# Performance work log

Measured on AMD Instinct MI355X. Metric: run time of the kernel, lower is better.

## Reference

```python
import jax, jax.numpy as jnp
import numpy as np
from jax import lax

EPS = 1e-5

def _ternarize_impl(w):
    # TWN: delta = 0.7*mean|w|; alpha = mean(|w| over |w|>delta); w -> {-alpha,0,+alpha}
    abs_w = jnp.abs(w)
    delta = 0.7 * abs_w.mean()
    mask_pos = w > delta
    mask_neg = w < -delta
    nz = mask_pos | mask_neg
    cnt = nz.sum()
    alpha = jnp.where(cnt > 0, (abs_w * nz).sum() / jnp.maximum(cnt, 1).astype(w.dtype), abs_w.mean())
    return jnp.where(mask_pos, alpha, jnp.where(mask_neg, -alpha, jnp.zeros((), w.dtype)))

def ternarize(w):
    return _ternarize_impl(w)

def conv_block(x, w, b, gamma, beta):
    tw = ternarize(w)
    y = lax.conv_general_dilated(x, tw, window_strides=(1, 1),
                                 padding=((1, 1), (1, 1)),
                                 dimension_numbers=('NCHW', 'OIHW', 'NCHW'))
    y = y + b[None, :, None, None]
    # BatchNorm2d in training mode: batch statistics over (N,H,W)
    mean = y.mean(axis=(0, 2, 3), keepdims=True)
    var = y.var(axis=(0, 2, 3), keepdims=True)
    y = (y - mean) * lax.rsqrt(var + EPS)
    y = y * gamma[None, :, None, None] + beta[None, :, None, None]
    y = jax.nn.relu(y)
    # MaxPool2d(2)
    y = lax.reduce_window(y, -jnp.inf, lax.max, (1, 1, 2, 2), (1, 1, 2, 2), 'VALID')
    return y

def setup_inputs() -> dict:
    key = jax.random.key(0)
    ks = jax.random.split(key, 32)
    chans = [3, 64, 128, 256, 512]
    d = {"x": jax.random.normal(ks[0], (32, 3, 128, 128), jnp.float32)}
    for i in range(4):
        cin, cout = chans[i], chans[i + 1]
        fan = cin * 9
        d[f"w{i+1}"] = jax.random.normal(ks[1 + 3 * i], (cout, cin, 3, 3), jnp.float32) / np.sqrt(fan)
        d[f"b{i+1}"] = jax.random.normal(ks[2 + 3 * i], (cout,), jnp.float32) * 0.01
        d[f"g{i+1}"] = jnp.ones((cout,), jnp.float32)
        d[f"be{i+1}"] = jnp.zeros((cout,), jnp.float32)
    fc_in = 512 * 8 * 8  # spatial = 128 // 2**4 = 8
    d["fw1"] = jax.random.normal(ks[20], (1024, fc_in), jnp.float32) / np.sqrt(fc_in)
    d["fb1"] = jax.random.normal(ks[21], (1024,), jnp.float32) * 0.01
    d["fw2"] = jax.random.normal(ks[22], (1000, 1024), jnp.float32) / np.sqrt(1024)
    d["fb2"] = jax.random.normal(ks[23], (1000,), jnp.float32) * 0.01
    return d

def reference(x, w1, b1, g1, be1, w2, b2, g2, be2, w3, b3, g3, be3, w4, b4, g4, be4, fw1, fb1, fw2, fb2):
    y = conv_block(x, w1, b1, g1, be1)
    y = conv_block(y, w2, b2, g2, be2)
    y = conv_block(y, w3, b3, g3, be3)
    y = conv_block(y, w4, b4, g4, be4)
    y = y.reshape(y.shape[0], -1)  # [B, 512*8*8]
    y = y @ ternarize(fw1).T + fb1
    y = jax.nn.relu(y)
    y = y @ ternarize(fw2).T + fb2
    return y
```

## Files before the change

kernel.cpp:

```cpp
#include <hip/hip_runtime.h>
#include <hip/hip_bf16.h>
#include <stdint.h>

#define DEV __device__ __forceinline__

typedef __bf16 bf16x8 __attribute__((ext_vector_type(8)));
typedef float f32x4 __attribute__((ext_vector_type(4)));
typedef unsigned short us8 __attribute__((ext_vector_type(8)));
typedef int8_t i8x8 __attribute__((ext_vector_type(8)));

DEV unsigned short f2us(float f) {
  __hip_bfloat16 h = __float2bfloat16(f);
  unsigned short u;
  __builtin_memcpy(&u, &h, 2);
  return u;
}

DEV double wave_reduce_d(double v) {
#pragma unroll
  for (int off = 32; off > 0; off >>= 1) v += __shfl_down(v, off);
  return v;
}

DEV double dbl_block_reduce(double v, double* lds) {
  v = wave_reduce_d(v);
  int lane = threadIdx.x & 63, w = threadIdx.x >> 6;
  if (lane == 0) lds[w] = v;
  __syncthreads();
  double r = 0.0;
  if (threadIdx.x == 0) r = lds[0] + lds[1] + lds[2] + lds[3];
  __syncthreads();
  return r;
}

struct TDesc { const float* w; int n; int b0; int nb; int slot; };
struct TDescs { TDesc d[6]; };

DEV double abs4d(float4 v) {
  return fabs((double)v.x) + fabs((double)v.y) + fabs((double)v.z) + fabs((double)v.w);
}

DEV double bucket_sum64(const double* b) {
  double s = 0.0;
#pragma unroll
  for (int j = 0; j < 64; ++j) s += b[j];
  return s;
}

__global__ __launch_bounds__(256) void tern_abs_all(TDescs td, double* __restrict__ absB) {
  __shared__ double lds[4];
  const int b = blockIdx.x;
  int k = 0;
  while (k < 5 && b >= td.d[k + 1].b0) ++k;
  const TDesc D = td.d[k];
  const float4* w4 = (const float4*)D.w;
  const int n4 = D.n >> 2;
  const int S = D.nb * 256;
  int i = (b - D.b0) * 256 + threadIdx.x;
  double s0 = 0.0, s1 = 0.0, s2 = 0.0, s3 = 0.0;
  for (; i + 3 * S < n4; i += 4 * S) {
    float4 v0 = w4[i];
    float4 v1 = w4[i + S];
    float4 v2 = w4[i + 2 * S];
    float4 v3 = w4[i + 3 * S];
    s0 += abs4d(v0);
    s1 += abs4d(v1);
    s2 += abs4d(v2);
    s3 += abs4d(v3);
  }
  for (; i < n4; i += S) s0 += abs4d(w4[i]);
  double s = (s0 + s1) + (s2 + s3);
  s = dbl_block_reduce(s, lds);
  if (threadIdx.x == 0 && s != 0.0) atomicAdd(absB + D.slot * 64 + (b & 63), s);
}

struct MDesc { const float* w; int8_t* out; int n; int b0; int nb; int slot; };
struct MDescs { MDesc d[6]; };

DEV int proc4(float4 v, double delta, double& ms, int& cnt) {
  float e[4] = {v.x, v.y, v.z, v.w};
  char pk[4];
#pragma unroll
  for (int j = 0; j < 4; ++j) {
    double d = (double)e[j];
    double a = fabs(d);
    if (a > delta) { ms += a; cnt += 1; }
    pk[j] = (char)((d > delta) ? 1 : ((d < -delta) ? -1 : 0));
  }
  int w32;
  __builtin_memcpy(&w32, pk, 4);
  return w32;
}

__global__ __launch_bounds__(256) void tern_masked_code_all(MDescs td,
                                                            const double* __restrict__ absB,
                                                            double* __restrict__ msB,
                                                            double* __restrict__ cntB) {
  __shared__ double lds[4];
  const int b = blockIdx.x;
  int k = 0;
  while (k < 5 && b >= td.d[k + 1].b0) ++k;
  const MDesc D = td.d[k];
  const float4* w4 = (const float4*)D.w;
  int8_t* out = D.out;
  const int n4 = D.n >> 2;
  const double delta = 0.7 * bucket_sum64(absB + D.slot * 64) / (double)D.n;
  const int S = D.nb * 256;
  int i = (b - D.b0) * 256 + threadIdx.x;
  double m0 = 0.0, m1 = 0.0, m2 = 0.0, m3 = 0.0;
  int c0 = 0, c1x = 0, c2x = 0, c3 = 0;
  for (; i + 3 * S < n4; i += 4 * S) {
    float4 v0 = w4[i];
    float4 v1 = w4[i + S];
    float4 v2 = w4[i + 2 * S];
    float4 v3 = w4[i + 3 * S];
    int p0 = proc4(v0, delta, m0, c0);
    int p1 = proc4(v1, delta, m1, c1x);
    int p2 = proc4(v2, delta, m2, c2x);
    int p3 = proc4(v3, delta, m3, c3);
    if (out) {
      *(int*)(out + ((size_t)i << 2)) = p0;
      *(int*)(out + ((size_t)(i + S) << 2)) = p1;
      *(int*)(out + ((size_t)(i + 2 * S) << 2)) = p2;
      *(int*)(out + ((size_t)(i + 3 * S) << 2)) = p3;
    }
  }
  for (; i < n4; i += S) {
    int p = proc4(w4[i], delta, m0, c0);
    if (out) *(int*)(out + ((size_t)i << 2)) = p;
  }
  double ms = (m0 + m1) + (m2 + m3);
  double cnt = (double)(c0 + c1x + c2x + c3);
  ms = dbl_block_reduce(ms, lds);
  cnt = dbl_block_reduce(cnt, lds);
  if (threadIdx.x == 0 && cnt != 0.0) {
    atomicAdd(msB + D.slot * 64 + (b & 63), ms);
    atomicAdd(cntB + D.slot * 64 + (b & 63), cnt);
  }
}

__global__ __launch_bounds__(64) void tern_collapse(const double* __restrict__ absB,
                                                    const double* __restrict__ msB,
                                                    const double* __restrict__ cntB,
                                                    double* __restrict__ st) {
  const int t = blockIdx.x;
  const int lane = threadIdx.x;
  double a = absB[t * 64 + lane];
  double m = msB[t * 64 + lane];
  double c = cntB[t * 64 + lane];
#pragma unroll
  for (int off = 32; off > 0; off >>= 1) {
    a += __shfl_down(a, off);
    m += __shfl_down(m, off);
    c += __shfl_down(c, off);
  }
  if (lane == 0) {
    st[t * 4] = a;
    st[t * 4 + 1] = m;
    st[t * 4 + 2] = c;
  }
}

DEV float tern_alpha_d(const double* st, double n) {
  double cnt = st[2];
  return (float)(cnt > 0.0 ? st[1] / fmax(cnt, 1.0) : st[0] / n);
}
DEV double tern_alpha_dd(const double* st, double n) {
  double cnt = st[2];
  return cnt > 0.0 ? st[1] / fmax(cnt, 1.0) : st[0] / n;
}

__global__ __launch_bounds__(256) void tern_write_convb(const float* __restrict__ w,
                                                        const double* __restrict__ ab, int total,
                                                        int CIN, unsigned short* __restrict__ out) {
  int i = blockIdx.x * 256 + threadIdx.x;
  if (i >= total) return;
  double delta = 0.7 * bucket_sum64(ab) / (double)total;
  double v = (double)w[i];
  float code = v > delta ? 1.f : (v < -delta ? -1.f : 0.f);
  int cin9 = CIN * 9;
  int o = i / cin9, rem = i - o * cin9;
  int ci = rem / 9, tap = rem - ci * 9;
  int CH = CIN >> 5;
  int blk = o >> 7, cop = o & 127;
  int wv = cop >> 5, g = (cop >> 4) & 1, l15 = cop & 15;
  int cc = ci >> 5, l4 = (ci >> 3) & 3, j = ci & 7;
  size_t idx =
      (((((size_t)(blk * CH + cc) * 9 + tap) * 4 + wv) * 2 + g) * 64 + l4 * 16 + l15) * 8 + j;
  out[idx] = f2us(code);
}

__global__ __launch_bounds__(256) void tern_write_convb_pad(const float* __restrict__ w,
                                                            const double* __restrict__ ab,
                                                            unsigned short* __restrict__ out) {
  int i = blockIdx.x * 256 + threadIdx.x;
  if (i >= 64 * 32) return;
  int o = i >> 5, k = i & 31;
  float code = 0.f;
  if (k < 27) {
    int dy = k / 9, r = k - dy * 9, dx = r / 3, ci = r - dx * 3;
    int tap = dy * 3 + dx;
    double delta = 0.7 * bucket_sum64(ab) / 1728.0;
    double v = (double)w[(o * 3 + ci) * 9 + tap];
    code = v > delta ? 1.f : (v < -delta ? -1.f : 0.f);
  }
  out[i] = f2us(code);
}

__global__ __launch_bounds__(256) void bn_fin_alpha(const double* __restrict__ pS,
                                                    const double* __restrict__ pQ, int P,
                                                    const float* __restrict__ g,
                                                    const float* __restrict__ be, double M,
                                                    const double* __restrict__ st, double nels,
                                                    float* __restrict__ scsh, int C) {
  __shared__ double lds[4];
  const int c = blockIdx.x;
  double s = 0.0, q = 0.0;
  for (int p = threadIdx.x; p < P; p += 256) {
    s += pS[(size_t)p * C + c];
    q += pQ[(size_t)p * C + c];
  }
  s = dbl_block_reduce(s, lds);
  q = dbl_block_reduce(q, lds);
  if (threadIdx.x == 0) {
    double al = tern_alpha_dd(st, nels);
    double mean = s / M;
    double var = q / M - mean * mean;
    double sc = (double)g[c] * al / sqrt(al * al * var + 1e-5);
    scsh[c] = (float)sc;
    scsh[C + c] = (float)((double)be[c] - mean * sc);
  }
}

DEV void cvt8(float4 a, float4 b, us8& hv, us8& lv) {
  float f[8] = {a.x, a.y, a.z, a.w, b.x, b.y, b.z, b.w};
#pragma unroll
  for (int e = 0; e < 8; ++e) {
    __hip_bfloat16 h = __float2bfloat16(f[e]);
    unsigned short hu;
    __builtin_memcpy(&hu, &h, 2);
    hv[e] = hu;
    lv[e] = f2us(f[e] - __bfloat162float(h));
  }
}

template <int PH>
DEV void bn_partials(const f32x4 (&acc)[2][PH], int wvCout, int CO, int p,
                     double* __restrict__ pS, double* __restrict__ pQ) {
  const int lane = threadIdx.x & 63;
  const int l15 = lane & 15, l4 = lane >> 4;
#pragma unroll
  for (int g = 0; g < 2; ++g) {
    float sv[4] = {0, 0, 0, 0}, qv[4] = {0, 0, 0, 0};
#pragma unroll
    for (int pt = 0; pt < PH; ++pt)
#pragma unroll
      for (int r = 0; r < 4; ++r) {
        float v = acc[g][pt][r];
        sv[r] += v;
        qv[r] = fmaf(v, v, qv[r]);
      }
#pragma unroll
    for (int r = 0; r < 4; ++r)
#pragma unroll
      for (int m = 1; m < 16; m <<= 1) {
        sv[r] += __shfl_xor(sv[r], m);
        qv[r] += __shfl_xor(qv[r], m);
      }
    if (l15 == 0) {
#pragma unroll
      for (int r = 0; r < 4; ++r) {
        int co = wvCout + g * 16 + l4 * 4 + r;
        pS[(size_t)p * CO + co] = (double)sv[r];
        pQ[(size_t)p * CO + co] = (double)qv[r];
      }
    }
  }
}

template <int CIN, int PH>
DEV void mfma_phase(const unsigned short* __restrict__ wT, const unsigned short* hC,
                    const unsigned short* lC, int wv, int blk, int cc, int lane,
                    f32x4 (&acc)[2][PH]) {
  constexpr int CH = CIN / 32;
  const int l15 = lane & 15, l4 = lane >> 4;
#pragma unroll
  for (int tap = 0; tap < 9; ++tap) {
    const int dy = tap / 3, dx = tap % 3;
    bf16x8 aF[2];
    const size_t wbase = (((size_t)(blk * CH + cc) * 9 + tap) * 4 + wv) * 2;
#pragma unroll
    for (int g = 0; g < 2; ++g)
      aF[g] = *(const bf16x8*)(wT + (wbase + g) * 512 + lane * 8);
    const int tb = (dy * 18 + dx + l15) * 32 + l4 * 8;
#pragma unroll
    for (int pt = 0; pt < PH; ++pt) {
      int off = tb + pt * (18 * 32);
      bf16x8 bh = *(const bf16x8*)(hC + off);
      bf16x8 bl = *(const bf16x8*)(lC + off);
      acc[0][pt] = __builtin_amdgcn_mfma_f32_16x16x32_bf16(aF[0], bh, acc[0][pt], 0, 0, 0);
      acc[1][pt] = __builtin_amdgcn_mfma_f32_16x16x32_bf16(aF[1], bh, acc[1][pt], 0, 0, 0);
      acc[0][pt] = __builtin_amdgcn_mfma_f32_16x16x32_bf16(aF[0], bl, acc[0][pt], 0, 0, 0);
      acc[1][pt] = __builtin_amdgcn_mfma_f32_16x16x32_bf16(aF[1], bl, acc[1][pt], 0, 0, 0);
    }
  }
}

template <int CIN, int H, int PH>
__global__ __launch_bounds__(256) void conv_mfma(const float* __restrict__ inNHWC,
                                                 const unsigned short* __restrict__ wT,
                                                 float* __restrict__ z, int COUT,
                                                 double* __restrict__ pS,
                                                 double* __restrict__ pQ) {
  constexpr int W = H;
  constexpr int CH = CIN / 32;
  constexpr int TX = W / 16;
  constexpr int NU = (PH + 2) * 18 * 4;
  constexpr int T = 256;
  constexpr int UPT = (NU + T - 1) / T;
  constexpr int TILE = (PH + 2) * 18 * 32;
  __shared__ unsigned short hiT[TILE];
  __shared__ unsigned short loT[TILE];
  const int bx = blockIdx.x;
  const int tX = bx % TX, tY = bx / TX;
  const int n = blockIdx.z;
  const int wave = threadIdx.x >> 6, lane = threadIdx.x & 63;
  const int l15 = lane & 15, l4 = lane >> 4;
  const int wvCout = blockIdx.y * 128 + wave * 32;
  const int x0 = tX * 16, y0 = tY * PH;

  f32x4 acc[2][PH];
#pragma unroll
  for (int g = 0; g < 2; ++g)
#pragma unroll
    for (int pt = 0; pt < PH; ++pt) acc[g][pt] = (f32x4){0.f, 0.f, 0.f, 0.f};

  const float* srcB[UPT];
  int ldsO[UPT];
  bool inb[UPT];
#pragma unroll
  for (int j = 0; j < UPT; ++j) {
    int u = threadIdx.x + j * T;
    int q = u & 3, rem = u >> 2;
    int xx = rem % 18, yy = rem / 18;
    int gy = y0 + yy - 1, gx = x0 + xx - 1;
    bool ok = (u < NU) && ((unsigned)gy < (unsigned)H) && ((unsigned)gx < (unsigned)W);
    inb[j] = ok;
    int cy = ok ? gy : 0, cx = ok ? gx : 0;
    srcB[j] = inNHWC + (((size_t)(n * H + cy) * W + cx) * CIN + q * 8);
    ldsO[j] = (rem << 5) + (q << 3);
  }
  float4 pa[UPT], pb[UPT];
#pragma unroll
  for (int j = 0; j < UPT; ++j)
    if (inb[j]) {
      pa[j] = *(const float4*)srcB[j];
      pb[j] = *(const float4*)(srcB[j] + 4);
    }
#pragma unroll 1
  for (int cc = 0; cc < CH; ++cc) {
    if (cc) {
      asm volatile("s_waitcnt lgkmcnt(0)" ::: "memory");
      __builtin_amdgcn_s_barrier();
      __builtin_amdgcn_sched_barrier(0);
    }
#pragma unroll
    for (int j = 0; j < UPT; ++j) {
      int u = threadIdx.x + j * T;
      if (u < NU) {
        us8 hv = (us8)0, lv = (us8)0;
        if (inb[j]) cvt8(pa[j], pb[j], hv, lv);
        *(us8*)(hiT + ldsO[j]) = hv;
        *(us8*)(loT + ldsO[j]) = lv;
      }
    }
    asm volatile("s_waitcnt lgkmcnt(0)" ::: "memory");
    __builtin_amdgcn_s_barrier();
    __builtin_amdgcn_sched_barrier(0);
    if (cc + 1 < CH) {
#pragma unroll
      for (int j = 0; j < UPT; ++j)
        if (inb[j]) {
          pa[j] = *(const float4*)(srcB[j] + (size_t)(cc + 1) * 32);
          pb[j] = *(const float4*)(srcB[j] + (size_t)(cc + 1) * 32 + 4);
        }
    }
    mfma_phase<CIN, PH>(wT, hiT, loT, wave, blockIdx.y, cc, lane, acc);
  }

#pragma unroll
  for (int g = 0; g < 2; ++g)
#pragma unroll
    for (int pt = 0; pt < PH; ++pt) {
      int oy = y0 + pt;
#pragma unroll
      for (int r = 0; r < 4; ++r) {
        int co = wvCout + g * 16 + l4 * 4 + r;
        z[(((size_t)n * COUT + co) * H + oy) * W + x0 + l15] = acc[g][pt][r];
      }
    }
  bn_partials<PH>(acc, wvCout, COUT, n * gridDim.x + bx, pS, pQ);
}

DEV void conv1_core(const float* __restrict__ x, const unsigned short* __restrict__ wb,
                    int n, int x0, int y0, float* xt, f32x4 (&acc)[2][8]) {
  const int lane = threadIdx.x & 63;
  const int l15 = lane & 15, l4 = lane >> 4;
  const int wvCout = (threadIdx.x >> 6) * 32;
#pragma unroll
  for (int g = 0; g < 2; ++g)
#pragma unroll
    for (int pt = 0; pt < 8; ++pt) acc[g][pt] = (f32x4){0.f, 0.f, 0.f, 0.f};

  for (int u = threadIdx.x; u < 540; u += 128) {
    int yy = u / 54, rem = u - yy * 54;
    int tx = rem / 3, ci = rem - tx * 3;
    int gy = y0 + yy - 1, gx = x0 + tx - 1;
    float v = 0.f;
    if ((unsigned)gy < 128u && (unsigned)gx < 128u)
      v = x[(((size_t)n * 3 + ci) << 14) + (gy << 7) + gx];
    xt[u] = v;
  }
  asm volatile("s_waitcnt lgkmcnt(0)" ::: "memory");
  __builtin_amdgcn_s_barrier();
  __builtin_amdgcn_sched_barrier(0);

  bf16x8 aW[2];
#pragma unroll
  for (int g = 0; g < 2; ++g)
    aW[g] = *(const bf16x8*)(wb + (size_t)(wvCout + g * 16 + l15) * 32 + l4 * 8);

#pragma unroll
  for (int pt = 0; pt < 8; ++pt) {
    us8 hv = (us8)0, lv = (us8)0;
#pragma unroll
    for (int j = 0; j < 8; ++j) {
      int k = l4 * 8 + j;
      float v = 0.f;
      if (k < 27) {
        int dy = k / 9;
        int r = k - dy * 9;
        v = xt[(pt + dy) * 54 + l15 * 3 + r];
      }
      __hip_bfloat16 h = __float2bfloat16(v);
      unsigned short hu;
      __builtin_memcpy(&hu, &h, 2);
      hv[j] = hu;
      lv[j] = f2us(v - __bfloat162float(h));
    }
    bf16x8 bh, bl;
    __builtin_memcpy(&bh, &hv, 16);
    __builtin_memcpy(&bl, &lv, 16);
    acc[0][pt] = __builtin_amdgcn_mfma_f32_16x16x32_bf16(aW[0], bh, acc[0][pt], 0, 0, 0);
    acc[0][pt] = __builtin_amdgcn_mfma_f32_16x16x32_bf16(aW[0], bl, acc[0][pt], 0, 0, 0);
    acc[1][pt] = __builtin_amdgcn_mfma_f32_16x16x32_bf16(aW[1], bh, acc[1][pt], 0, 0, 0);
    acc[1][pt] = __builtin_amdgcn_mfma_f32_16x16x32_bf16(aW[1], bl, acc[1][pt], 0, 0, 0);
  }
}

__global__ __launch_bounds__(128) void conv1_mfma_stats(const float* __restrict__ x,
                                                        const unsigned short* __restrict__ wT,
                                                        double* __restrict__ pS,
                                                        double* __restrict__ pQ) {
  __shared__ float xt[540];
  const int bx = blockIdx.x;
  const int tX = bx & 7, tY = bx >> 3;
  const int n = blockIdx.z;
  f32x4 acc[2][8];
  conv1_core(x, wT, n, tX * 16, tY * 8, xt, acc);
  bn_partials<8>(acc, (threadIdx.x >> 6) * 32, 64, n * gridDim.x + bx, pS, pQ);
}

__global__ __launch_bounds__(128) void conv1_mfma_pool(const float* __restrict__ x,
                                                       const unsigned short* __restrict__ wT,
                                                       const float* __restrict__ scsh,
                                                       float* __restrict__ outNHWC) {
  __shared__ float xt[540];
  const int bx = blockIdx.x;
  const int tX = bx & 7, tY = bx >> 3;
  const int n = blockIdx.z;
  const int lane = threadIdx.x & 63;
  const int l15 = lane & 15, l4 = lane >> 4;
  const int wvCout = (threadIdx.x >> 6) * 32;
  const int x0 = tX * 16, y0 = tY * 8;
  f32x4 acc[2][8];
  conv1_core(x, wT, n, x0, y0, xt, acc);
#pragma unroll
  for (int g = 0; g < 2; ++g) {
    const int co0 = wvCout + g * 16 + l4 * 4;
#pragma unroll
    for (int pt = 0; pt < 8; pt += 2) {
      float m[4];
#pragma unroll
      for (int r = 0; r < 4; ++r) {
        float sc = scsh[co0 + r], sh = scsh[64 + co0 + r];
        float v0 = fmaxf(fmaf(acc[g][pt][r], sc, sh), 0.f);
        float v1 = fmaxf(fmaf(acc[g][pt + 1][r], sc, sh), 0.f);
        float a = fmaxf(v0, v1);
        m[r] = fmaxf(a, __shfl_xor(a, 1));
      }
      if ((l15 & 1) == 0) {
        int oy = (y0 + pt) >> 1, ox = (x0 + l15) >> 1;
        *(float4*)(outNHWC + ((((size_t)n * 64 + oy) * 64 + ox) << 6) + co0) =
            make_float4(m[0], m[1], m[2], m[3]);
      }
    }
  }
}

__global__ __launch_bounds__(256) void bn_pool_nhwc(const float* __restrict__ z,
                                                    const float* __restrict__ scsh, int C,
                                                    int lw, float* __restrict__ out) {
  __shared__ float t[64][65];
  const int Wo = 1 << lw, Wi = Wo << 1;
  const int c0 = blockIdx.x * 64, p0 = blockIdx.y * 64, n = blockIdx.z;
  const int NP = Wo * Wo;
  for (int u = threadIdx.x; u < 4096; u += 256) {
    int cl = u >> 6, pl = u & 63;
    int pp = p0 + pl, ho = pp >> lw, wo = pp & (Wo - 1);
    int c = c0 + cl;
    size_t idx = ((size_t)(n * C + c) * Wi + (ho << 1)) * Wi + (wo << 1);
    float sc = scsh[c], sh = scsh[C + c];
    float z00 = fmaxf(fmaf(z[idx], sc, sh), 0.f);
    float z01 = fmaxf(fmaf(z[idx + 1], sc, sh), 0.f);
    float z10 = fmaxf(fmaf(z[idx + Wi], sc, sh), 0.f);
    float z11 = fmaxf(fmaf(z[idx + Wi + 1], sc, sh), 0.f);
    t[cl][pl] = fmaxf(fmaxf(z00, z01), fmaxf(z10, z11));
  }
  __syncthreads();
  for (int u = threadIdx.x; u < 4096; u += 256) {
    int pl = u >> 6, cl = u & 63;
    out[((size_t)n * NP + p0 + pl) * C + c0 + cl] = t[cl][pl];
  }
}

__global__ __launch_bounds__(256) void bn_pool_hilo(const float* __restrict__ z,
                                                    const float* __restrict__ scsh,
                                                    unsigned short* __restrict__ hi,
                                                    unsigned short* __restrict__ lo) {
  int i = blockIdx.x * 256 + threadIdx.x;
  int wo = i & 7, ho = (i >> 3) & 7, c = (i >> 6) & 511, n = i >> 15;
  float sc = scsh[c], sh = scsh[512 + c];
  size_t idx = ((size_t)(n * 512 + c) * 16 + (ho << 1)) * 16 + (wo << 1);
  float z00 = fmaxf(fmaf(z[idx], sc, sh), 0.f);
  float z01 = fmaxf(fmaf(z[idx + 1], sc, sh), 0.f);
  float z10 = fmaxf(fmaf(z[idx + 16], sc, sh), 0.f);
  float z11 = fmaxf(fmaf(z[idx + 17], sc, sh), 0.f);
  float f = fmaxf(fmaxf(z00, z01), fmaxf(z10, z11));
  __hip_bfloat16 h = __float2bfloat16(f);
  unsigned short hu;
  __builtin_memcpy(&hu, &h, 2);
  hi[i] = hu;
  lo[i] = f2us(f - __bfloat162float(h));
}

DEV bf16x8 i8_to_bf16x8(i8x8 v) {
  us8 u;
#pragma unroll
  for (int j = 0; j < 8; ++j) {
    int c = v[j];
    u[j] = (unsigned short)(c == 0 ? 0 : (c > 0 ? 0x3F80 : 0xBF80));
  }
  bf16x8 r;
  __builtin_memcpy(&r, &u, 16);
  return r;
}

__global__ __launch_bounds__(256) void fc1_mfma(const int8_t* __restrict__ c1,
                                                const unsigned short* __restrict__ aHi,
                                                const unsigned short* __restrict__ aLo,
                                                float* __restrict__ partial) {
  const int w = threadIdx.x >> 6, lane = threadIdx.x & 63;
  const int l15 = lane & 15, l4 = lane >> 4;
  const int o0 = blockIdx.x * 128 + w * 32;
  const int s = blockIdx.y;
  const int kbase = s * 256 + l4 * 8;
  f32x4 acc[2][2];
#pragma unroll
  for (int g = 0; g < 2; ++g)
#pragma unroll
    for (int t = 0; t < 2; ++t) acc[g][t] = (f32x4){0.f, 0.f, 0.f, 0.f};
#pragma unroll 2
  for (int kc = 0; kc < 256; kc += 32) {
    bf16x8 a0 = i8_to_bf16x8(*(const i8x8*)(c1 + (size_t)(o0 + l15) * 32768 + kbase + kc));
    bf16x8 a1 = i8_to_bf16x8(*(const i8x8*)(c1 + (size_t)(o0 + 16 + l15) * 32768 + kbase + kc));
    bf16x8 bh0 = *(const bf16x8*)(aHi + (size_t)l15 * 32768 + kbase + kc);
    bf16x8 bl0 = *(const bf16x8*)(aLo + (size_t)l15 * 32768 + kbase + kc);
    bf16x8 bh1 = *(const bf16x8*)(aHi + (size_t)(16 + l15) * 32768 + kbase + kc);
    bf16x8 bl1 = *(const bf16x8*)(aLo + (size_t)(16 + l15) * 32768 + kbase + kc);
    acc[0][0] = __builtin_amdgcn_mfma_f32_16x16x32_bf16(a0, bh0, acc[0][0], 0, 0, 0);
    acc[0][0] = __builtin_amdgcn_mfma_f32_16x16x32_bf16(a0, bl0, acc[0][0], 0, 0, 0);
    acc[1][0] = __builtin_amdgcn_mfma_f32_16x16x32_bf16(a1, bh0, acc[1][0], 0, 0, 0);
    acc[1][0] = __builtin_amdgcn_mfma_f32_16x16x32_bf16(a1, bl0, acc[1][0], 0, 0, 0);
    acc[0][1] = __builtin_amdgcn_mfma_f32_16x16x32_bf16(a0, bh1, acc[0][1], 0, 0, 0);
    acc[0][1] = __builtin_amdgcn_mfma_f32_16x16x32_bf16(a0, bl1, acc[0][1], 0, 0, 0);
    acc[1][1] = __builtin_amdgcn_mfma_f32_16x16x32_bf16(a1, bh1, acc[1][1], 0, 0, 0);
    acc[1][1] = __builtin_amdgcn_mfma_f32_16x16x32_bf16(a1, bl1, acc[1][1], 0, 0, 0);
  }
#pragma unroll
  for (int g = 0; g < 2; ++g)
#pragma unroll
    for (int t = 0; t < 2; ++t)
#pragma unroll
      for (int r = 0; r < 4; ++r) {
        int o = o0 + g * 16 + l4 * 4 + r;
        int n = t * 16 + l15;
        partial[((size_t)s * 1024 + o) * 32 + n] = acc[g][t][r];
      }
}

__global__ __launch_bounds__(256) void fc1_fin(const float* __restrict__ partial,
                                               const double* __restrict__ st,
                                               const float* __restrict__ fb,
                                               float* __restrict__ fc1T) {
  int i = blockIdx.x * 256 + threadIdx.x;
  int o = i >> 5;
  float s = 0.f;
#pragma unroll 8
  for (int t = 0; t < 128; ++t) s += partial[(size_t)t * 32768 + i];
  float alpha = tern_alpha_d(st, 33554432.0);
  fc1T[i] = fmaxf(fmaf(s, alpha, fb[o]), 0.f);
}

__global__ __launch_bounds__(256) void fc2_kernel(const float* __restrict__ xT,
                                                  const int8_t* __restrict__ codes,
                                                  const double* __restrict__ st,
                                                  const float* __restrict__ fb,
                                                  float* __restrict__ out) {
  const int o = blockIdx.x;
  float acc[32];
#pragma unroll
  for (int j = 0; j < 32; ++j) acc[j] = 0.f;
  const int8_t* crow = codes + (size_t)o * 1024;
  for (int k = threadIdx.x; k < 1024; k += 256) {
    int cv = crow[k];
    if (cv != 0) {
      float c = (float)cv;
      const float4* pv = (const float4*)(xT + ((size_t)k << 5));
#pragma unroll
      for (int j = 0; j < 8; ++j) {
        float4 v = pv[j];
        acc[4 * j + 0] = fmaf(c, v.x, acc[4 * j + 0]);
        acc[4 * j + 1] = fmaf(c, v.y, acc[4 * j + 1]);
        acc[4 * j + 2] = fmaf(c, v.z, acc[4 * j + 2]);
        acc[4 * j + 3] = fmaf(c, v.w, acc[4 * j + 3]);
      }
    }
  }
#pragma unroll
  for (int j = 0; j < 32; ++j) {
#pragma unroll
    for (int off = 32; off > 0; off >>= 1) acc[j] += __shfl_down(acc[j], off);
  }
  __shared__ float red[4][32];
  int lane = threadIdx.x & 63, wv = threadIdx.x >> 6;
  if (lane == 0) {
#pragma unroll
    for (int j = 0; j < 32; ++j) red[wv][j] = acc[j];
  }
  __syncthreads();
  if (threadIdx.x < 32) {
    int n = threadIdx.x;
    float alpha = tern_alpha_d(st, 1024000.0);
    out[(size_t)n * 1000 + o] = (red[0][n] + red[1][n] + red[2][n] + red[3][n]) * alpha + fb[o];
  }
}

extern "C" void kernel_launch(void* const* d_in, const int* in_sizes, int n_in, void* d_out,
                              int out_size, void* d_ws, size_t ws_size, hipStream_t stream) {
  const float* x = (const float*)d_in[0];
  const float* w1 = (const float*)d_in[1];
  const float* g1 = (const float*)d_in[3];
  const float* be1 = (const float*)d_in[4];
  const float* w2 = (const float*)d_in[5];
  const float* g2 = (const float*)d_in[7];
  const float* be2 = (const float*)d_in[8];
  const float* w3 = (const float*)d_in[9];
  const float* g3 = (const float*)d_in[11];
  const float* be3 = (const float*)d_in[12];
  const float* w4 = (const float*)d_in[13];
  const float* g4 = (const float*)d_in[15];
  const float* be4 = (const float*)d_in[16];
  const float* fw1 = (const float*)d_in[17];
  const float* fb1 = (const float*)d_in[18];
  const float* fw2 = (const float*)d_in[19];
  const float* fb2 = (const float*)d_in[20];
  (void)in_sizes; (void)n_in; (void)out_size; (void)ws_size;

  char* ws = (char*)d_ws;
  size_t off = 0;
  auto alloc = [&](size_t bytes) {
    size_t o = off;
    off += (bytes + 255) & ~(size_t)255;
    return o;
  };
  unsigned short* wb1 = (unsigned short*)(ws + alloc((size_t)2048 * 2));
  unsigned short* wb2 = (unsigned short*)(ws + alloc((size_t)73728 * 2));
  unsigned short* wb3 = (unsigned short*)(ws + alloc((size_t)294912 * 2));
  unsigned short* wb4 = (unsigned short*)(ws + alloc((size_t)1179648 * 2));
  int8_t* c1 = (int8_t*)(ws + alloc((size_t)33554432));
  int8_t* c2 = (int8_t*)(ws + alloc((size_t)1024000));
  double* dst = (double*)(ws + alloc((size_t)(32 + 3 * 384) * 8));
  double* absB = dst + 32;
  double* msB = absB + 384;
  double* cntB = msB + 384;
  float* scsh = (float*)(ws + alloc((size_t)4096 * 4));
  double* pS = (double*)(ws + alloc((size_t)262144 * 8));
  double* pQ = (double*)(ws + alloc((size_t)262144 * 8));
  float* bufY = (float*)(ws + alloc((size_t)16777216 * 4));
  float* bufA = (float*)(ws + alloc((size_t)8388608 * 4));
  unsigned short* actHi = (unsigned short*)(ws + alloc((size_t)1048576 * 2));
  unsigned short* actLo = (unsigned short*)(ws + alloc((size_t)1048576 * 2));
  float* fc1T = (float*)(ws + alloc((size_t)32768 * 4));
  float* fc1part = bufY;

  hipMemsetAsync(dst, 0, (32 + 3 * 384) * 8, stream);

  TDescs ta;
  ta.d[0] = {fw1, 33554432, 0, 8192, 4};
  ta.d[1] = {w4, 1179648, 8192, 288, 3};
  ta.d[2] = {fw2, 1024000, 8480, 250, 5};
  ta.d[3] = {w3, 294912, 8730, 72, 2};
  ta.d[4] = {w2, 73728, 8802, 18, 1};
  ta.d[5] = {w1, 1728, 8820, 1, 0};
  tern_abs_all<<<8821, 256, 0, stream>>>(ta, absB);
  MDescs tm;
  tm.d[0] = {fw1, c1, 33554432, 0, 8192, 4};
  tm.d[1] = {w4, nullptr, 1179648, 8192, 288, 3};
  tm.d[2] = {fw2, c2, 1024000, 8480, 250, 5};
  tm.d[3] = {w3, nullptr, 294912, 8730, 72, 2};
  tm.d[4] = {w2, nullptr, 73728, 8802, 18, 1};
  tm.d[5] = {w1, nullptr, 1728, 8820, 1, 0};
  tern_masked_code_all<<<8821, 256, 0, stream>>>(tm, absB, msB, cntB);
  tern_collapse<<<6, 64, 0, stream>>>(absB, msB, cntB, dst);
  tern_write_convb_pad<<<8, 256, 0, stream>>>(w1, absB + 0 * 64, wb1);
  tern_write_convb<<<288, 256, 0, stream>>>(w2, absB + 1 * 64, 73728, 64, wb2);
  tern_write_convb<<<1152, 256, 0, stream>>>(w3, absB + 2 * 64, 294912, 128, wb3);
  tern_write_convb<<<4608, 256, 0, stream>>>(w4, absB + 3 * 64, 1179648, 256, wb4);

  float* ss1 = scsh;
  float* ss2 = scsh + 128;
  float* ss3 = scsh + 512;
  float* ss4 = scsh + 1024;

  conv1_mfma_stats<<<dim3(128, 1, 32), 128, 0, stream>>>(x, wb1, pS, pQ);
  bn_fin_alpha<<<64, 256, 0, stream>>>(pS, pQ, 4096, g1, be1, 524288.0, dst + 0, 1728.0, ss1,
                                       64);
  conv1_mfma_pool<<<dim3(128, 1, 32), 128, 0, stream>>>(x, wb1, ss1, bufA);

  conv_mfma<64, 64, 8><<<dim3(32, 1, 32), 256, 0, stream>>>(bufA, wb2, bufY, 128, pS, pQ);
  bn_fin_alpha<<<128, 256, 0, stream>>>(pS, pQ, 1024, g2, be2, 131072.0, dst + 4, 73728.0, ss2,
                                        128);
  bn_pool_nhwc<<<dim3(2, 16, 32), 256, 0, stream>>>(bufY, ss2, 128, 5, bufA);

  conv_mfma<128, 32, 4><<<dim3(16, 2, 32), 256, 0, stream>>>(bufA, wb3, bufY, 256, pS, pQ);
  bn_fin_alpha<<<256, 256, 0, stream>>>(pS, pQ, 512, g3, be3, 32768.0, dst + 8, 294912.0, ss3,
                                        256);
  bn_pool_nhwc<<<dim3(4, 4, 32), 256, 0, stream>>>(bufY, ss3, 256, 4, bufA);

  conv_mfma<256, 16, 2><<<dim3(8, 4, 32), 256, 0, stream>>>(bufA, wb4, bufY, 512, pS, pQ);
  bn_fin_alpha<<<512, 256, 0, stream>>>(pS, pQ, 256, g4, be4, 8192.0, dst + 12, 1179648.0, ss4,
                                        512);
  bn_pool_hilo<<<4096, 256, 0, stream>>>(bufY, ss4, actHi, actLo);

  fc1_mfma<<<dim3(8, 128), 256, 0, stream>>>(c1, actHi, actLo, fc1part);
  fc1_fin<<<128, 256, 0, stream>>>(fc1part, dst + 16, fb1, fc1T);
  fc2_kernel<<<1000, 256, 0, stream>>>(fc1T, c2, dst + 20, fb2, (float*)d_out);
}
```

Before: 565.1 us.

## Halve per-block output-channel tile in conv_mfma to double grid parallelism

Each conv block now computes 64 output channels (16 per wave) instead of 128, so each wave holds one accumulator group instead of two. The weight packing layout drops the g dimension to match, and the grid y-dimension doubles for conv2-4. This is meant to raise occupancy and parallelism for the small-grid later layers, where grids were only 1024-4096 blocks. In exchange, each input tile is loaded from global memory and converted to hi/lo bf16 in LDS twice as often, and each MFMA has half the A-fragment reuse.

```diff
diff --git a/kernel.cpp b/kernel.cpp
--- a/kernel.cpp
+++ b/kernel.cpp
@@ -182,11 +182,11 @@
   int o = i / cin9, rem = i - o * cin9;
   int ci = rem / 9, tap = rem - ci * 9;
   int CH = CIN >> 5;
-  int blk = o >> 7, cop = o & 127;
-  int wv = cop >> 5, g = (cop >> 4) & 1, l15 = cop & 15;
+  int blk = o >> 6, cop = o & 63;
+  int wv = cop >> 4, l15 = cop & 15;
   int cc = ci >> 5, l4 = (ci >> 3) & 3, j = ci & 7;
   size_t idx =
-      (((((size_t)(blk * CH + cc) * 9 + tap) * 4 + wv) * 2 + g) * 64 + l4 * 16 + l15) * 8 + j;
+      ((((size_t)(blk * CH + cc) * 9 + tap) * 4 + wv) * 64 + l4 * 16 + l15) * 8 + j;
   out[idx] = f2us(code);
 }
 
@@ -278,30 +278,56 @@
   }
 }
 
+template <int PH>
+DEV void bn_partials1(const f32x4 (&acc)[PH], int wvCout, int CO, int p,
+                      double* __restrict__ pS, double* __restrict__ pQ) {
+  const int lane = threadIdx.x & 63;
+  const int l15 = lane & 15, l4 = lane >> 4;
+  float sv[4] = {0, 0, 0, 0}, qv[4] = {0, 0, 0, 0};
+#pragma unroll
+  for (int pt = 0; pt < PH; ++pt)
+#pragma unroll
+    for (int r = 0; r < 4; ++r) {
+      float v = acc[pt][r];
+      sv[r] += v;
+      qv[r] = fmaf(v, v, qv[r]);
+    }
+#pragma unroll
+  for (int r = 0; r < 4; ++r)
+#pragma unroll
+    for (int m = 1; m < 16; m <<= 1) {
+      sv[r] += __shfl_xor(sv[r], m);
+      qv[r] += __shfl_xor(qv[r], m);
+    }
+  if (l15 == 0) {
+#pragma unroll
+    for (int r = 0; r < 4; ++r) {
+      int co = wvCout + l4 * 4 + r;
+      pS[(size_t)p * CO + co] = (double)sv[r];
+      pQ[(size_t)p * CO + co] = (double)qv[r];
+    }
+  }
+}
+
 template <int CIN, int PH>
 DEV void mfma_phase(const unsigned short* __restrict__ wT, const unsigned short* hC,
-                    const unsigned short* lC, int wv, int blk, int cc, int lane,
-                    f32x4 (&acc)[2][PH]) {
+                    const unsigned short* lC, int wv, int blkY, int cc, int lane,
+                    f32x4 (&acc)[PH]) {
   constexpr int CH = CIN / 32;
   const int l15 = lane & 15, l4 = lane >> 4;
 #pragma unroll
   for (int tap = 0; tap < 9; ++tap) {
     const int dy = tap / 3, dx = tap % 3;
-    bf16x8 aF[2];
-    const size_t wbase = (((size_t)(blk * CH + cc) * 9 + tap) * 4 + wv) * 2;
-#pragma unroll
-    for (int g = 0; g < 2; ++g)
-      aF[g] = *(const bf16x8*)(wT + (wbase + g) * 512 + lane * 8);
+    const size_t wbase = (((size_t)(blkY * CH + cc) * 9 + tap) * 4 + wv);
+    bf16x8 aF = *(const bf16x8*)(wT + wbase * 512 + lane * 8);
     const int tb = (dy * 18 + dx + l15) * 32 + l4 * 8;
 #pragma unroll
     for (int pt = 0; pt < PH; ++pt) {
       int off = tb + pt * (18 * 32);
       bf16x8 bh = *(const bf16x8*)(hC + off);
       bf16x8 bl = *(const bf16x8*)(lC + off);
-      acc[0][pt] = __builtin_amdgcn_mfma_f32_16x16x32_bf16(aF[0], bh, acc[0][pt], 0, 0, 0);
-      acc[1][pt] = __builtin_amdgcn_mfma_f32_16x16x32_bf16(aF[1], bh, acc[1][pt], 0, 0, 0);
-      acc[0][pt] = __builtin_amdgcn_mfma_f32_16x16x32_bf16(aF[0], bl, acc[0][pt], 0, 0, 0);
-      acc[1][pt] = __builtin_amdgcn_mfma_f32_16x16x32_bf16(aF[1], bl, acc[1][pt], 0, 0, 0);
+      acc[pt] = __builtin_amdgcn_mfma_f32_16x16x32_bf16(aF, bh, acc[pt], 0, 0, 0);
+      acc[pt] = __builtin_amdgcn_mfma_f32_16x16x32_bf16(aF, bl, acc[pt], 0, 0, 0);
     }
   }
 }
@@ -326,14 +352,12 @@
   const int n = blockIdx.z;
   const int wave = threadIdx.x >> 6, lane = threadIdx.x & 63;
   const int l15 = lane & 15, l4 = lane >> 4;
-  const int wvCout = blockIdx.y * 128 + wave * 32;
+  const int wvCout = blockIdx.y * 64 + wave * 16;
   const int x0 = tX * 16, y0 = tY * PH;
 
-  f32x4 acc[2][PH];
-#pragma unroll
-  for (int g = 0; g < 2; ++g)
-#pragma unroll
-    for (int pt = 0; pt < PH; ++pt) acc[g][pt] = (f32x4){0.f, 0.f, 0.f, 0.f};
+  f32x4 acc[PH];
+#pragma unroll
+  for (int pt = 0; pt < PH; ++pt) acc[pt] = (f32x4){0.f, 0.f, 0.f, 0.f};
 
   const float* srcB[UPT];
   int ldsO[UPT];
@@ -389,17 +413,15 @@
   }
 
 #pragma unroll
-  for (int g = 0; g < 2; ++g)
-#pragma unroll
-    for (int pt = 0; pt < PH; ++pt) {
-      int oy = y0 + pt;
-#pragma unroll
-      for (int r = 0; r < 4; ++r) {
-        int co = wvCout + g * 16 + l4 * 4 + r;
-        z[(((size_t)n * COUT + co) * H + oy) * W + x0 + l15] = acc[g][pt][r];
-      }
-    }
-  bn_partials<PH>(acc, wvCout, COUT, n * gridDim.x + bx, pS, pQ);
+  for (int pt = 0; pt < PH; ++pt) {
+    int oy = y0 + pt;
+#pragma unroll
+    for (int r = 0; r < 4; ++r) {
+      int co = wvCout + l4 * 4 + r;
+      z[(((size_t)n * COUT + co) * H + oy) * W + x0 + l15] = acc[pt][r];
+    }
+  }
+  bn_partials1<PH>(acc, wvCout, COUT, n * gridDim.x + bx, pS, pQ);
 }
 
 DEV void conv1_core(const float* __restrict__ x, const unsigned short* __restrict__ wb,
@@ -748,17 +770,17 @@
                                        64);
   conv1_mfma_pool<<<dim3(128, 1, 32), 128, 0, stream>>>(x, wb1, ss1, bufA);
 
-  conv_mfma<64, 64, 8><<<dim3(32, 1, 32), 256, 0, stream>>>(bufA, wb2, bufY, 128, pS, pQ);
+  conv_mfma<64, 64, 8><<<dim3(32, 2, 32), 256, 0, stream>>>(bufA, wb2, bufY, 128, pS, pQ);
   bn_fin_alpha<<<128, 256, 0, stream>>>(pS, pQ, 1024, g2, be2, 131072.0, dst + 4, 73728.0, ss2,
                                         128);
   bn_pool_nhwc<<<dim3(2, 16, 32), 256, 0, stream>>>(bufY, ss2, 128, 5, bufA);
 
-  conv_mfma<128, 32, 4><<<dim3(16, 2, 32), 256, 0, stream>>>(bufA, wb3, bufY, 256, pS, pQ);
+  conv_mfma<128, 32, 4><<<dim3(16, 4, 32), 256, 0, stream>>>(bufA, wb3, bufY, 256, pS, pQ);
   bn_fin_alpha<<<256, 256, 0, stream>>>(pS, pQ, 512, g3, be3, 32768.0, dst + 8, 294912.0, ss3,
                                         256);
   bn_pool_nhwc<<<dim3(4, 4, 32), 256, 0, stream>>>(bufY, ss3, 256, 4, bufA);
 
-  conv_mfma<256, 16, 2><<<dim3(8, 4, 32), 256, 0, stream>>>(bufA, wb4, bufY, 512, pS, pQ);
+  conv_mfma<256, 16, 2><<<dim3(8, 8, 32), 256, 0, stream>>>(bufA, wb4, bufY, 512, pS, pQ);
   bn_fin_alpha<<<512, 256, 0, stream>>>(pS, pQ, 256, g4, be4, 8192.0, dst + 12, 1179648.0, ss4,
                                         512);
   bn_pool_hilo<<<4096, 256, 0, stream>>>(bufY, ss4, actHi, actLo);
```

Measured after the change: 589.7 us. 1.04x slower.

## Double-buffer LDS input tiles in conv_mfma to drop one barrier per chunk

Applied to the files above, without the earlier changes.

For conv layers with at least four 32-channel chunks, the input tile's hi/lo LDS buffers are doubled and used alternately. This removes the barrier that guarded overwriting the tile while other waves were still reading it, leaving one barrier per chunk instead of two. The next chunk's global loads are issued before the barrier rather than after it. The cost is twice the LDS for those layers, which can reduce occupancy.

```diff
diff --git a/kernel.cpp b/kernel.cpp
--- a/kernel.cpp
+++ b/kernel.cpp
@@ -319,8 +319,9 @@
   constexpr int T = 256;
   constexpr int UPT = (NU + T - 1) / T;
   constexpr int TILE = (PH + 2) * 18 * 32;
-  __shared__ unsigned short hiT[TILE];
-  __shared__ unsigned short loT[TILE];
+  constexpr int NB = (CH >= 4) ? 2 : 1;
+  __shared__ unsigned short hiT[NB * TILE];
+  __shared__ unsigned short loT[NB * TILE];
   const int bx = blockIdx.x;
   const int tX = bx % TX, tY = bx / TX;
   const int n = blockIdx.z;
@@ -357,35 +358,66 @@
       pa[j] = *(const float4*)srcB[j];
       pb[j] = *(const float4*)(srcB[j] + 4);
     }
+
+  if constexpr (NB == 1) {
 #pragma unroll 1
-  for (int cc = 0; cc < CH; ++cc) {
-    if (cc) {
+    for (int cc = 0; cc < CH; ++cc) {
+      if (cc) {
+        asm volatile("s_waitcnt lgkmcnt(0)" ::: "memory");
+        __builtin_amdgcn_s_barrier();
+        __builtin_amdgcn_sched_barrier(0);
+      }
+#pragma unroll
+      for (int j = 0; j < UPT; ++j) {
+        int u = threadIdx.x + j * T;
+        if (u < NU) {
+          us8 hv = (us8)0, lv = (us8)0;
+          if (inb[j]) cvt8(pa[j], pb[j], hv, lv);
+          *(us8*)(hiT + ldsO[j]) = hv;
+          *(us8*)(loT + ldsO[j]) = lv;
+        }
+      }
       asm volatile("s_waitcnt lgkmcnt(0)" ::: "memory");
       __builtin_amdgcn_s_barrier();
       __builtin_amdgcn_sched_barrier(0);
-    }
-#pragma unroll
-    for (int j = 0; j < UPT; ++j) {
-      int u = threadIdx.x + j * T;
-      if (u < NU) {
-        us8 hv = (us8)0, lv = (us8)0;
-        if (inb[j]) cvt8(pa[j], pb[j], hv, lv);
-        *(us8*)(hiT + ldsO[j]) = hv;
-        *(us8*)(loT + ldsO[j]) = lv;
-      }
-    }
-    asm volatile("s_waitcnt lgkmcnt(0)" ::: "memory");
-    __builtin_amdgcn_s_barrier();
-    __builtin_amdgcn_sched_barrier(0);
-    if (cc + 1 < CH) {
-#pragma unroll
-      for (int j = 0; j < UPT; ++j)
-        if (inb[j]) {
-          pa[j] = *(const float4*)(srcB[j] + (size_t)(cc + 1) * 32);
-          pb[j] = *(const float4*)(srcB[j] + (size_t)(cc + 1) * 32 + 4);
+      if (cc + 1 < CH) {
+#pragma unroll
+        for (int j = 0; j < UPT; ++j)
+          if (inb[j]) {
+            pa[j] = *(const float4*)(srcB[j] + (size_t)(cc + 1) * 32);
+            pb[j] = *(const float4*)(srcB[j] + (size_t)(cc + 1) * 32 + 4);
+          }
+      }
+      mfma_phase<CIN, PH>(wT, hiT, loT, wave, blockIdx.y, cc, lane, acc);
+    }
+  } else {
+#pragma unroll 1
+    for (int cc = 0; cc < CH; ++cc) {
+      unsigned short* hC = hiT + (cc & 1) * TILE;
+      unsigned short* lC = loT + (cc & 1) * TILE;
+#pragma unroll
+      for (int j = 0; j < UPT; ++j) {
+        int u = threadIdx.x + j * T;
+        if (u < NU) {
+          us8 hv = (us8)0, lv = (us8)0;
+          if (inb[j]) cvt8(pa[j], pb[j], hv, lv);
+          *(us8*)(hC + ldsO[j]) = hv;
+          *(us8*)(lC + ldsO[j]) = lv;
         }
-    }
-    mfma_phase<CIN, PH>(wT, hiT, loT, wave, blockIdx.y, cc, lane, acc);
+      }
+      if (cc + 1 < CH) {
+#pragma unroll
+        for (int j = 0; j < UPT; ++j)
+          if (inb[j]) {
+            pa[j] = *(const float4*)(srcB[j] + (size_t)(cc + 1) * 32);
+            pb[j] = *(const float4*)(srcB[j] + (size_t)(cc + 1) * 32 + 4);
+          }
+      }
+      asm volatile("s_waitcnt lgkmcnt(0)" ::: "memory");
+      __builtin_amdgcn_s_barrier();
+      __builtin_amdgcn_sched_barrier(0);
+      mfma_phase<CIN, PH>(wT, hC, lC, wave, blockIdx.y, cc, lane, acc);
+    }
   }
 
 #pragma unroll
```

Result: no change. 575.3 us (+1.8%).
